# Kernel optimization log

Measured on AMD Instinct MI355X. Metric: run time of the kernel, lower is better.

## Reference

```python
import jax, jax.numpy as jnp
import numpy as np

T, B, D, Hd = 512, 64, 1024, 1024
SIGMA = 0.01


def setup_inputs() -> dict:
    key = jax.random.key(0)
    ks = jax.random.split(key, 9)
    inp = {
        "inputs": jax.random.normal(ks[0], (T, B, D), dtype=jnp.float32),
        "H0": jnp.zeros((B, Hd), dtype=jnp.float32),
        "C0": jnp.zeros((B, Hd), dtype=jnp.float32),
    }
    names_x = ["W_xi", "W_xf", "W_xo", "W_xc"]
    names_h = ["W_hi", "W_hf", "W_ho", "W_hc"]
    for i, n in enumerate(names_x):
        inp[n] = jax.random.normal(ks[1 + i], (D, Hd), dtype=jnp.float32) * SIGMA
    for i, n in enumerate(names_h):
        inp[n] = jax.random.normal(ks[5 + i], (Hd, Hd), dtype=jnp.float32) * SIGMA
    for n in ["b_i", "b_f", "b_o", "b_c"]:
        inp[n] = jnp.zeros((Hd,), dtype=jnp.float32)
    return inp


def reference(inputs, H0, C0, W_xi, W_xf, W_xo, W_xc,
              W_hi, W_hf, W_ho, W_hc, b_i, b_f, b_o, b_c):
    # Fuse the 4 input-projection and 4 hidden-projection GEMMs into 2 GEMMs
    # per step (same math as 8 separate matmuls, just concatenated).
    Wx = jnp.concatenate([W_xi, W_xf, W_xo, W_xc], axis=1)   # [D, 4H]
    Wh = jnp.concatenate([W_hi, W_hf, W_ho, W_hc], axis=1)   # [H, 4H]
    b = jnp.concatenate([b_i, b_f, b_o, b_c], axis=0)        # [4H]
    nh = b_i.shape[0]

    def step(carry, X):
        H, C = carry
        gates = X @ Wx + H @ Wh + b                          # [B, 4H]
        i, f, o, g = jnp.split(gates, 4, axis=1)
        I = jax.nn.sigmoid(i)
        F = jax.nn.sigmoid(f)
        O = jax.nn.sigmoid(o)
        C_tilde = jnp.tanh(g)
        C_new = F * C + I * C_tilde
        H_new = O * jnp.tanh(C_new)
        return (H_new, C_new), H_new

    (H_f, C_f), outputs = jax.lax.scan(step, (H0, C0), inputs)  # outputs [T, B, H]
    return outputs, (H_f, C_f)
```

## Files before the change

### kernel.cpp

```cpp
#include <hip/hip_runtime.h>
#include <cstdint>

#define TT 512
#define BB 64
#define DD 1024
#define HH 1024
#define NWG 128

typedef __attribute__((ext_vector_type(8))) __bf16 bf16x8;
typedef __attribute__((ext_vector_type(4))) float f32x4;

#define WS_XQ    0
#define WS_WHB   67108864ULL
#define WS_HQ    83886080ULL
#define WS_FLAGS 151126016ULL
#define FLAGS_BYTES ((TT + 1) * NWG * 4)

__device__ __forceinline__ unsigned short f2bf(float f) {
    unsigned int u = __float_as_uint(f);
    u = (u + 0x7fffu + ((u >> 16) & 1u)) >> 16;
    return (unsigned short)u;
}

__device__ __forceinline__ float sigm(float x) {
    return 1.0f / (1.0f + __expf(-x));
}
__device__ __forceinline__ float tanh_f(float x) {
    float a = fabsf(x);
    float e = __expf(-2.0f * a);
    float t = (1.0f - e) / (1.0f + e);
    return copysignf(t, x);
}

__device__ __forceinline__ unsigned long long pack4bf(float a, float b, float c, float d) {
    return (unsigned long long)f2bf(a)
         | ((unsigned long long)f2bf(b) << 16)
         | ((unsigned long long)f2bf(c) << 32)
         | ((unsigned long long)f2bf(d) << 48);
}

__global__ void cvt_x(const float* __restrict__ X, unsigned short* __restrict__ Xq) {
    int i = blockIdx.x * blockDim.x + threadIdx.x;
    const int n8 = TT * BB * DD / 8;
    if (i >= n8) return;
    const float4* s = (const float4*)X;
    float4 a = s[2 * i], b = s[2 * i + 1];
    union { unsigned short u[8]; uint4 q; } r;
    r.u[0] = f2bf(a.x); r.u[1] = f2bf(a.y); r.u[2] = f2bf(a.z); r.u[3] = f2bf(a.w);
    r.u[4] = f2bf(b.x); r.u[5] = f2bf(b.y); r.u[6] = f2bf(b.z); r.u[7] = f2bf(b.w);
    ((uint4*)Xq)[i] = r.q;
}

__global__ void pack_w(const float* __restrict__ Wxi, const float* __restrict__ Wxf,
                       const float* __restrict__ Wxo, const float* __restrict__ Wxc,
                       const float* __restrict__ Whi, const float* __restrict__ Whf,
                       const float* __restrict__ Who, const float* __restrict__ Whc,
                       unsigned short* __restrict__ WhB) {
    int tid = blockIdx.x * blockDim.x + threadIdx.x;
    int lane = tid & 63;
    int ct   = (tid >> 6) & 1;
    int s    = (tid >> 7) & 15;
    int kq   = (tid >> 11) & 3;
    int wg   = tid >> 13;
    int col  = ct * 16 + (lane & 15);
    int gate = col >> 3;
    int h    = wg * 8 + (col & 7);
    int kb   = kq * 512 + s * 32 + ((lane >> 4) & 3) * 8;

    const float* Wx[4] = {Wxi, Wxf, Wxo, Wxc};
    const float* Wh[4] = {Whi, Whf, Who, Whc};
    const float* W = (kb < 1024) ? (Wx[gate] + (size_t)kb * HH + h)
                                 : (Wh[gate] + (size_t)(kb - 1024) * HH + h);
    union { unsigned short u[8]; uint4 q; } r;
#pragma unroll
    for (int m = 0; m < 8; ++m) r.u[m] = f2bf(W[(size_t)m * HH]);
    *(uint4*)(WhB + (size_t)tid * 8) = r.q;
}

__global__ void __launch_bounds__(512, 2)
lstm_seq(const unsigned short* __restrict__ Xq, const unsigned short* __restrict__ WhB,
         unsigned short* __restrict__ Hq, int* flags,
         const float* __restrict__ H0, const float* __restrict__ C0,
         const float* __restrict__ bi, const float* __restrict__ bfp,
         const float* __restrict__ bo, const float* __restrict__ bc,
         float* __restrict__ out) {
    __shared__ float gpart[4][64][37];
    __shared__ int hs;

    const int wg    = blockIdx.x;
    const int tid   = threadIdx.x;
    const int wv    = tid >> 6;
    const int lane  = tid & 63;
    const int quad  = lane >> 4;
    const int l15   = lane & 15;
    const int rhalf = wv & 1;
    const bool isH  = (wv >= 4);
    const int kq    = isH ? 2 + ((wv - 4) >> 1) : (wv >> 1);
    const int arow0 = rhalf * 32 + l15;

    const bool isAct = (wv == 4) || (wv == 5);
    const int aidx   = tid - 256;
    const int r2     = aidx >> 1;
    const int ahalf  = aidx & 1;
    const int hcol0  = wg * 8 + ahalf * 4;

    float Bi[4], Bf[4], Bo[4], Bc[4], Cr[4];
    if (isAct) {
#pragma unroll
        for (int j = 0; j < 4; ++j) {
            Bi[j] = bi[hcol0 + j];
            Bf[j] = bfp[hcol0 + j];
            Bo[j] = bo[hcol0 + j];
            Bc[j] = bc[hcol0 + j];
            Cr[j] = C0[(size_t)r2 * HH + hcol0 + j];
        }
    }

    bf16x8 Breg[16][2];
    {
        const unsigned short* wp = WhB + (size_t)(wg * 4 + kq) * (16 * 2 * 64 * 8);
#pragma unroll
        for (int s = 0; s < 16; ++s)
#pragma unroll
            for (int ct = 0; ct < 2; ++ct)
                Breg[s][ct] = *(const bf16x8*)(wp + ((s * 2 + ct) * 64 + lane) * 8);
    }

    if (tid == 0) hs = 0;
    if (tid < 64) {
        const float* s = H0 + (size_t)tid * HH + wg * 8;
        unsigned long long a = pack4bf(s[0], s[1], s[2], s[3]);
        unsigned long long b = pack4bf(s[4], s[5], s[6], s[7]);
        unsigned long long* d = (unsigned long long*)(Hq + (size_t)tid * HH + wg * 8);
        __hip_atomic_store(d,     a, __ATOMIC_RELAXED, __HIP_MEMORY_SCOPE_AGENT);
        __hip_atomic_store(d + 1, b, __ATOMIC_RELAXED, __HIP_MEMORY_SCOPE_AGENT);
    }
    __syncthreads();
    if (tid == 0)
        __hip_atomic_store(&flags[wg], 1, __ATOMIC_RELAXED, __HIP_MEMORY_SCOPE_AGENT);

    for (int t = 0; t < TT; ++t) {
        f32x4 a00 = {0.f,0.f,0.f,0.f}, a01 = {0.f,0.f,0.f,0.f};
        f32x4 a10 = {0.f,0.f,0.f,0.f}, a11 = {0.f,0.f,0.f,0.f};

        if (!isH) {
            const unsigned short* xb = Xq + ((size_t)(t * BB + arow0)) * DD + kq * 512 + quad * 8;
#pragma unroll
            for (int s = 0; s < 16; ++s) {
                bf16x8 af0 = *(const bf16x8*)(xb + s * 32);
                bf16x8 af1 = *(const bf16x8*)(xb + 16 * DD + s * 32);
                a00 = __builtin_amdgcn_mfma_f32_16x16x32_bf16(af0, Breg[s][0], a00, 0, 0, 0);
                a01 = __builtin_amdgcn_mfma_f32_16x16x32_bf16(af0, Breg[s][1], a01, 0, 0, 0);
                a10 = __builtin_amdgcn_mfma_f32_16x16x32_bf16(af1, Breg[s][0], a10, 0, 0, 0);
                a11 = __builtin_amdgcn_mfma_f32_16x16x32_bf16(af1, Breg[s][1], a11, 0, 0, 0);
            }
        } else {
            const int kqh = kq - 2;
            const int* fp = flags + (size_t)t * NWG + kqh * 64 + lane;
            const unsigned short* hb = Hq + ((size_t)(t * BB + arow0)) * HH + kqh * 512 + quad * 8;
            int myf = 0;
            unsigned long long got = 0;

            while ((got & 0xFFFFFFFFull) != 0xFFFFFFFFull) {
                if (!myf) myf = __hip_atomic_load(fp, __ATOMIC_RELAXED, __HIP_MEMORY_SCOPE_AGENT);
                got = __ballot(myf != 0);
                if ((got & 0xFFFFFFFFull) != 0xFFFFFFFFull) __builtin_amdgcn_s_sleep(1);
            }
            asm volatile("" ::: "memory");
            bf16x8 af[8][2];
#pragma unroll
            for (int s = 0; s < 8; ++s) {
                af[s][0] = *(const bf16x8*)(hb + s * 32);
                af[s][1] = *(const bf16x8*)(hb + 16 * HH + s * 32);
            }
#pragma unroll
            for (int s = 0; s < 8; ++s) {
                a00 = __builtin_amdgcn_mfma_f32_16x16x32_bf16(af[s][0], Breg[s][0], a00, 0, 0, 0);
                a01 = __builtin_amdgcn_mfma_f32_16x16x32_bf16(af[s][0], Breg[s][1], a01, 0, 0, 0);
                a10 = __builtin_amdgcn_mfma_f32_16x16x32_bf16(af[s][1], Breg[s][0], a10, 0, 0, 0);
                a11 = __builtin_amdgcn_mfma_f32_16x16x32_bf16(af[s][1], Breg[s][1], a11, 0, 0, 0);
            }

            while (got != ~0ull) {
                if (!myf) myf = __hip_atomic_load(fp, __ATOMIC_RELAXED, __HIP_MEMORY_SCOPE_AGENT);
                got = __ballot(myf != 0);
                if (got != ~0ull) __builtin_amdgcn_s_sleep(1);
            }
            asm volatile("" ::: "memory");
#pragma unroll
            for (int s = 0; s < 8; ++s) {
                af[s][0] = *(const bf16x8*)(hb + (8 + s) * 32);
                af[s][1] = *(const bf16x8*)(hb + 16 * HH + (8 + s) * 32);
            }
#pragma unroll
            for (int s = 0; s < 8; ++s) {
                a00 = __builtin_amdgcn_mfma_f32_16x16x32_bf16(af[s][0], Breg[8 + s][0], a00, 0, 0, 0);
                a01 = __builtin_amdgcn_mfma_f32_16x16x32_bf16(af[s][0], Breg[8 + s][1], a01, 0, 0, 0);
                a10 = __builtin_amdgcn_mfma_f32_16x16x32_bf16(af[s][1], Breg[8 + s][0], a10, 0, 0, 0);
                a11 = __builtin_amdgcn_mfma_f32_16x16x32_bf16(af[s][1], Breg[8 + s][1], a11, 0, 0, 0);
            }
        }

#pragma unroll
        for (int r = 0; r < 4; ++r) {
            int row0 = rhalf * 32 + quad * 4 + r;
            gpart[kq][row0][l15]           = a00[r];
            gpart[kq][row0][16 + l15]      = a01[r];
            gpart[kq][row0 + 16][l15]      = a10[r];
            gpart[kq][row0 + 16][16 + l15] = a11[r];
        }
        __syncthreads();

        if (isAct) {
            float hv[4];
#pragma unroll
            for (int j = 0; j < 4; ++j) {
                const int c = ahalf * 4 + j;
                float gi = gpart[0][r2][c]      + gpart[1][r2][c]
                         + gpart[2][r2][c]      + gpart[3][r2][c]      + Bi[j];
                float gf = gpart[0][r2][8 + c]  + gpart[1][r2][8 + c]
                         + gpart[2][r2][8 + c]  + gpart[3][r2][8 + c]  + Bf[j];
                float go = gpart[0][r2][16 + c] + gpart[1][r2][16 + c]
                         + gpart[2][r2][16 + c] + gpart[3][r2][16 + c] + Bo[j];
                float gc = gpart[0][r2][24 + c] + gpart[1][r2][24 + c]
                         + gpart[2][r2][24 + c] + gpart[3][r2][24 + c] + Bc[j];
                float I = sigm(gi), F = sigm(gf), O = sigm(go), G = tanh_f(gc);
                Cr[j] = F * Cr[j] + I * G;
                hv[j] = O * tanh_f(Cr[j]);
            }
            unsigned long long pk = pack4bf(hv[0], hv[1], hv[2], hv[3]);
            __hip_atomic_store(
                (unsigned long long*)(Hq + ((size_t)(t + 1) * BB + r2) * HH + hcol0),
                pk, __ATOMIC_RELAXED, __HIP_MEMORY_SCOPE_AGENT);
            asm volatile("s_waitcnt vmcnt(0)" ::: "memory");
            if (lane == 0) {
                int prev = atomicAdd(&hs, 1);
                if (prev & 1)
                    __hip_atomic_store(flags + (size_t)(t + 1) * NWG + wg, 1,
                                       __ATOMIC_RELAXED, __HIP_MEMORY_SCOPE_AGENT);
            }
            float4 v = make_float4(hv[0], hv[1], hv[2], hv[3]);
            *(float4*)(out + ((size_t)t * BB + r2) * HH + hcol0) = v;
            if (t == TT - 1) {
                *(float4*)(out + (size_t)TT * BB * HH + (size_t)r2 * HH + hcol0) = v;
            }
        }
        __syncthreads();
    }

    if (isAct) {
        float* cf = out + (size_t)TT * BB * HH + (size_t)BB * HH;
        *(float4*)(cf + (size_t)r2 * HH + hcol0) = make_float4(Cr[0], Cr[1], Cr[2], Cr[3]);
    }
}

extern "C" void kernel_launch(void* const* d_in, const int* in_sizes, int n_in,
                              void* d_out, int out_size, void* d_ws, size_t ws_size,
                              hipStream_t stream) {
    const float* X   = (const float*)d_in[0];
    const float* H0  = (const float*)d_in[1];
    const float* C0  = (const float*)d_in[2];
    const float* Wxi = (const float*)d_in[3];
    const float* Wxf = (const float*)d_in[4];
    const float* Wxo = (const float*)d_in[5];
    const float* Wxc = (const float*)d_in[6];
    const float* Whi = (const float*)d_in[7];
    const float* Whf = (const float*)d_in[8];
    const float* Who = (const float*)d_in[9];
    const float* Whc = (const float*)d_in[10];
    const float* bi  = (const float*)d_in[11];
    const float* bf_ = (const float*)d_in[12];
    const float* bo  = (const float*)d_in[13];
    const float* bc  = (const float*)d_in[14];

    char* ws = (char*)d_ws;
    unsigned short* Xq  = (unsigned short*)(ws + WS_XQ);
    unsigned short* WhB = (unsigned short*)(ws + WS_WHB);
    unsigned short* Hq  = (unsigned short*)(ws + WS_HQ);
    int* flags          = (int*)(ws + WS_FLAGS);

    hipMemsetAsync(flags, 0, FLAGS_BYTES, stream);

    hipLaunchKernelGGL(cvt_x, dim3(TT * BB * DD / 8 / 256), dim3(256), 0, stream, X, Xq);
    hipLaunchKernelGGL(pack_w, dim3(4096), dim3(256), 0, stream,
                       Wxi, Wxf, Wxo, Wxc, Whi, Whf, Who, Whc, WhB);
    hipLaunchKernelGGL(lstm_seq, dim3(NWG), dim3(512), 0, stream,
                       Xq, WhB, Hq, flags, H0, C0, bi, bf_, bo, bc, (float*)d_out);
}
```

Measured before the change: 5.561 ms.

## Replace per-step flag handshake with sentinel-valued hidden-state polling

Removes the per-timestep flags array and its release protocol (waitcnt plus LDS counter plus flag store). Consumers instead poll the bf16 hidden-state words directly, using an all-ones sentinel written by a memset over the whole Hq buffer. This takes a store-then-flag round trip off the serial recurrence critical path. In exchange it adds a memset of about 67 MB before every launch and more atomic polling loads. It also relies on a valid h value never packing to the all-ones bit pattern, which is a NaN pattern in bf16.

```diff
diff --git a/kernel.cpp b/kernel.cpp
--- a/kernel.cpp
+++ b/kernel.cpp
@@ -13,8 +13,7 @@
 #define WS_XQ    0
 #define WS_WHB   67108864ULL
 #define WS_HQ    83886080ULL
-#define WS_FLAGS 151126016ULL
-#define FLAGS_BYTES ((TT + 1) * NWG * 4)
+#define HQ_BYTES ((size_t)(TT + 1) * BB * HH * 2)
 
 __device__ __forceinline__ unsigned short f2bf(float f) {
     unsigned int u = __float_as_uint(f);
@@ -79,13 +78,12 @@
 
 __global__ void __launch_bounds__(512, 2)
 lstm_seq(const unsigned short* __restrict__ Xq, const unsigned short* __restrict__ WhB,
-         unsigned short* __restrict__ Hq, int* flags,
+         unsigned short* __restrict__ Hq,
          const float* __restrict__ H0, const float* __restrict__ C0,
          const float* __restrict__ bi, const float* __restrict__ bfp,
          const float* __restrict__ bo, const float* __restrict__ bc,
          float* __restrict__ out) {
     __shared__ float gpart[4][64][37];
-    __shared__ int hs;
 
     const int wg    = blockIdx.x;
     const int tid   = threadIdx.x;
@@ -126,7 +124,6 @@
                 Breg[s][ct] = *(const bf16x8*)(wp + ((s * 2 + ct) * 64 + lane) * 8);
     }
 
-    if (tid == 0) hs = 0;
     if (tid < 64) {
         const float* s = H0 + (size_t)tid * HH + wg * 8;
         unsigned long long a = pack4bf(s[0], s[1], s[2], s[3]);
@@ -135,9 +132,8 @@
         __hip_atomic_store(d,     a, __ATOMIC_RELAXED, __HIP_MEMORY_SCOPE_AGENT);
         __hip_atomic_store(d + 1, b, __ATOMIC_RELAXED, __HIP_MEMORY_SCOPE_AGENT);
     }
-    __syncthreads();
-    if (tid == 0)
-        __hip_atomic_store(&flags[wg], 1, __ATOMIC_RELAXED, __HIP_MEMORY_SCOPE_AGENT);
+
+    const unsigned long long SENT = ~0ull;
 
     for (int t = 0; t < TT; ++t) {
         f32x4 a00 = {0.f,0.f,0.f,0.f}, a01 = {0.f,0.f,0.f,0.f};
@@ -156,48 +152,48 @@
             }
         } else {
             const int kqh = kq - 2;
-            const int* fp = flags + (size_t)t * NWG + kqh * 64 + lane;
             const unsigned short* hb = Hq + ((size_t)(t * BB + arow0)) * HH + kqh * 512 + quad * 8;
-            int myf = 0;
-            unsigned long long got = 0;
-
-            while ((got & 0xFFFFFFFFull) != 0xFFFFFFFFull) {
-                if (!myf) myf = __hip_atomic_load(fp, __ATOMIC_RELAXED, __HIP_MEMORY_SCOPE_AGENT);
-                got = __ballot(myf != 0);
-                if ((got & 0xFFFFFFFFull) != 0xFFFFFFFFull) __builtin_amdgcn_s_sleep(1);
-            }
-            asm volatile("" ::: "memory");
-            bf16x8 af[8][2];
-#pragma unroll
-            for (int s = 0; s < 8; ++s) {
-                af[s][0] = *(const bf16x8*)(hb + s * 32);
-                af[s][1] = *(const bf16x8*)(hb + 16 * HH + s * 32);
-            }
-#pragma unroll
-            for (int s = 0; s < 8; ++s) {
-                a00 = __builtin_amdgcn_mfma_f32_16x16x32_bf16(af[s][0], Breg[s][0], a00, 0, 0, 0);
-                a01 = __builtin_amdgcn_mfma_f32_16x16x32_bf16(af[s][0], Breg[s][1], a01, 0, 0, 0);
-                a10 = __builtin_amdgcn_mfma_f32_16x16x32_bf16(af[s][1], Breg[s][0], a10, 0, 0, 0);
-                a11 = __builtin_amdgcn_mfma_f32_16x16x32_bf16(af[s][1], Breg[s][1], a11, 0, 0, 0);
-            }
-
-            while (got != ~0ull) {
-                if (!myf) myf = __hip_atomic_load(fp, __ATOMIC_RELAXED, __HIP_MEMORY_SCOPE_AGENT);
-                got = __ballot(myf != 0);
-                if (got != ~0ull) __builtin_amdgcn_s_sleep(1);
-            }
-            asm volatile("" ::: "memory");
-#pragma unroll
-            for (int s = 0; s < 8; ++s) {
-                af[s][0] = *(const bf16x8*)(hb + (8 + s) * 32);
-                af[s][1] = *(const bf16x8*)(hb + 16 * HH + (8 + s) * 32);
-            }
-#pragma unroll
-            for (int s = 0; s < 8; ++s) {
-                a00 = __builtin_amdgcn_mfma_f32_16x16x32_bf16(af[s][0], Breg[8 + s][0], a00, 0, 0, 0);
-                a01 = __builtin_amdgcn_mfma_f32_16x16x32_bf16(af[s][0], Breg[8 + s][1], a01, 0, 0, 0);
-                a10 = __builtin_amdgcn_mfma_f32_16x16x32_bf16(af[s][1], Breg[8 + s][0], a10, 0, 0, 0);
-                a11 = __builtin_amdgcn_mfma_f32_16x16x32_bf16(af[s][1], Breg[8 + s][1], a11, 0, 0, 0);
+#pragma unroll
+            for (int p = 0; p < 2; ++p) {
+                unsigned long long vv[8][2][2];
+#pragma unroll
+                for (int s = 0; s < 8; ++s) {
+                    const unsigned long long* b0 =
+                        (const unsigned long long*)(hb + (p * 8 + s) * 32);
+                    const unsigned long long* b1 =
+                        (const unsigned long long*)(hb + 16 * HH + (p * 8 + s) * 32);
+                    vv[s][0][0] = __hip_atomic_load(b0,     __ATOMIC_RELAXED, __HIP_MEMORY_SCOPE_AGENT);
+                    vv[s][0][1] = __hip_atomic_load(b0 + 1, __ATOMIC_RELAXED, __HIP_MEMORY_SCOPE_AGENT);
+                    vv[s][1][0] = __hip_atomic_load(b1,     __ATOMIC_RELAXED, __HIP_MEMORY_SCOPE_AGENT);
+                    vv[s][1][1] = __hip_atomic_load(b1 + 1, __ATOMIC_RELAXED, __HIP_MEMORY_SCOPE_AGENT);
+                }
+                bool any;
+                do {
+                    any = false;
+#pragma unroll
+                    for (int s = 0; s < 8; ++s)
+#pragma unroll
+                        for (int rt = 0; rt < 2; ++rt)
+#pragma unroll
+                            for (int h = 0; h < 2; ++h)
+                                if (vv[s][rt][h] == SENT) {
+                                    const unsigned long long* b = (const unsigned long long*)
+                                        (hb + rt * 16 * HH + (p * 8 + s) * 32) + h;
+                                    vv[s][rt][h] = __hip_atomic_load(
+                                        b, __ATOMIC_RELAXED, __HIP_MEMORY_SCOPE_AGENT);
+                                    any = true;
+                                }
+                } while (any);
+#pragma unroll
+                for (int s = 0; s < 8; ++s) {
+                    union { unsigned long long u[2]; bf16x8 v; } f0, f1;
+                    f0.u[0] = vv[s][0][0]; f0.u[1] = vv[s][0][1];
+                    f1.u[0] = vv[s][1][0]; f1.u[1] = vv[s][1][1];
+                    a00 = __builtin_amdgcn_mfma_f32_16x16x32_bf16(f0.v, Breg[p*8+s][0], a00, 0, 0, 0);
+                    a01 = __builtin_amdgcn_mfma_f32_16x16x32_bf16(f0.v, Breg[p*8+s][1], a01, 0, 0, 0);
+                    a10 = __builtin_amdgcn_mfma_f32_16x16x32_bf16(f1.v, Breg[p*8+s][0], a10, 0, 0, 0);
+                    a11 = __builtin_amdgcn_mfma_f32_16x16x32_bf16(f1.v, Breg[p*8+s][1], a11, 0, 0, 0);
+                }
             }
         }
 
@@ -232,13 +228,6 @@
             __hip_atomic_store(
                 (unsigned long long*)(Hq + ((size_t)(t + 1) * BB + r2) * HH + hcol0),
                 pk, __ATOMIC_RELAXED, __HIP_MEMORY_SCOPE_AGENT);
-            asm volatile("s_waitcnt vmcnt(0)" ::: "memory");
-            if (lane == 0) {
-                int prev = atomicAdd(&hs, 1);
-                if (prev & 1)
-                    __hip_atomic_store(flags + (size_t)(t + 1) * NWG + wg, 1,
-                                       __ATOMIC_RELAXED, __HIP_MEMORY_SCOPE_AGENT);
-            }
             float4 v = make_float4(hv[0], hv[1], hv[2], hv[3]);
             *(float4*)(out + ((size_t)t * BB + r2) * HH + hcol0) = v;
             if (t == TT - 1) {
@@ -277,13 +266,12 @@
     unsigned short* Xq  = (unsigned short*)(ws + WS_XQ);
     unsigned short* WhB = (unsigned short*)(ws + WS_WHB);
     unsigned short* Hq  = (unsigned short*)(ws + WS_HQ);
-    int* flags          = (int*)(ws + WS_FLAGS);
-
-    hipMemsetAsync(flags, 0, FLAGS_BYTES, stream);
+
+    hipMemsetAsync(Hq, 0xFF, HQ_BYTES, stream);
 
     hipLaunchKernelGGL(cvt_x, dim3(TT * BB * DD / 8 / 256), dim3(256), 0, stream, X, Xq);
     hipLaunchKernelGGL(pack_w, dim3(4096), dim3(256), 0, stream,
                        Wxi, Wxf, Wxo, Wxc, Whi, Whf, Who, Whc, WhB);
     hipLaunchKernelGGL(lstm_seq, dim3(NWG), dim3(512), 0, stream,
-                       Xq, WhB, Hq, flags, H0, C0, bi, bf_, bo, bc, (float*)d_out);
-}
+                       Xq, WhB, Hq, H0, C0, bi, bf_, bo, bc, (float*)d_out);
+}
```

After: 6.924 ms. 24.5% more time.

## Use per-wave monotonic ring-buffer flags for finer-grained cross-workgroup step sync

Applied to the files above, without the earlier changes.

Each of the two activation waves now publishes its own flag, set to a monotonically increasing step value in an 8-slot ring padded to 16 bytes per flag. This replaces the shared-memory atomic counter that made the second wave publish for both. Consumer waves poll only the half of the rows they actually need, and compare against a step threshold instead of testing for nonzero. This shortens the critical path of the per-step cross-workgroup handoff and shrinks the flag buffer to clear. It also drops the gpart row padding from 37 to 36 and removes an initial __syncthreads, which risks LDS bank conflicts and relies on the ring never being lapped.

```diff
diff --git a/kernel.cpp b/kernel.cpp
--- a/kernel.cpp
+++ b/kernel.cpp
@@ -14,7 +14,7 @@
 #define WS_WHB   67108864ULL
 #define WS_HQ    83886080ULL
 #define WS_FLAGS 151126016ULL
-#define FLAGS_BYTES ((TT + 1) * NWG * 4)
+#define FLAGS_BYTES (256 * 128)
 
 __device__ __forceinline__ unsigned short f2bf(float f) {
     unsigned int u = __float_as_uint(f);
@@ -84,8 +84,7 @@
          const float* __restrict__ bi, const float* __restrict__ bfp,
          const float* __restrict__ bo, const float* __restrict__ bc,
          float* __restrict__ out) {
-    __shared__ float gpart[4][64][37];
-    __shared__ int hs;
+    __shared__ float gpart[4][64][36];
 
     const int wg    = blockIdx.x;
     const int tid   = threadIdx.x;
@@ -126,7 +125,6 @@
                 Breg[s][ct] = *(const bf16x8*)(wp + ((s * 2 + ct) * 64 + lane) * 8);
     }
 
-    if (tid == 0) hs = 0;
     if (tid < 64) {
         const float* s = H0 + (size_t)tid * HH + wg * 8;
         unsigned long long a = pack4bf(s[0], s[1], s[2], s[3]);
@@ -135,9 +133,12 @@
         __hip_atomic_store(d,     a, __ATOMIC_RELAXED, __HIP_MEMORY_SCOPE_AGENT);
         __hip_atomic_store(d + 1, b, __ATOMIC_RELAXED, __HIP_MEMORY_SCOPE_AGENT);
     }
-    __syncthreads();
-    if (tid == 0)
-        __hip_atomic_store(&flags[wg], 1, __ATOMIC_RELAXED, __HIP_MEMORY_SCOPE_AGENT);
+    if (wv == 0) {
+        asm volatile("s_waitcnt vmcnt(0)" ::: "memory");
+        if (lane < 2)
+            __hip_atomic_store(flags + ((wg * 2 + lane) * 8 + 0) * 4, 1,
+                               __ATOMIC_RELAXED, __HIP_MEMORY_SCOPE_AGENT);
+    }
 
     for (int t = 0; t < TT; ++t) {
         f32x4 a00 = {0.f,0.f,0.f,0.f}, a01 = {0.f,0.f,0.f,0.f};
@@ -155,49 +156,58 @@
                 a11 = __builtin_amdgcn_mfma_f32_16x16x32_bf16(af1, Breg[s][1], a11, 0, 0, 0);
             }
         } else {
-            const int kqh = kq - 2;
-            const int* fp = flags + (size_t)t * NWG + kqh * 64 + lane;
+            const int kqh  = kq - 2;
+            const int slot = t & 7;
+            const int thr  = t + 1;
+            const int* fp  = flags + (((kqh * 64 + lane) * 2 + rhalf) * 8 + slot) * 4;
             const unsigned short* hb = Hq + ((size_t)(t * BB + arow0)) * HH + kqh * 512 + quad * 8;
-            int myf = 0;
-            unsigned long long got = 0;
-
+
+            int myf = __hip_atomic_load(fp, __ATOMIC_RELAXED, __HIP_MEMORY_SCOPE_AGENT);
+            unsigned long long got = __ballot(myf >= thr);
             while ((got & 0xFFFFFFFFull) != 0xFFFFFFFFull) {
-                if (!myf) myf = __hip_atomic_load(fp, __ATOMIC_RELAXED, __HIP_MEMORY_SCOPE_AGENT);
-                got = __ballot(myf != 0);
-                if ((got & 0xFFFFFFFFull) != 0xFFFFFFFFull) __builtin_amdgcn_s_sleep(1);
+                __builtin_amdgcn_s_sleep(2);
+                if (myf < thr)
+                    myf = __hip_atomic_load(fp, __ATOMIC_RELAXED, __HIP_MEMORY_SCOPE_AGENT);
+                got = __ballot(myf >= thr);
             }
             asm volatile("" ::: "memory");
-            bf16x8 af[8][2];
-#pragma unroll
-            for (int s = 0; s < 8; ++s) {
-                af[s][0] = *(const bf16x8*)(hb + s * 32);
-                af[s][1] = *(const bf16x8*)(hb + 16 * HH + s * 32);
-            }
-#pragma unroll
-            for (int s = 0; s < 8; ++s) {
-                a00 = __builtin_amdgcn_mfma_f32_16x16x32_bf16(af[s][0], Breg[s][0], a00, 0, 0, 0);
-                a01 = __builtin_amdgcn_mfma_f32_16x16x32_bf16(af[s][0], Breg[s][1], a01, 0, 0, 0);
-                a10 = __builtin_amdgcn_mfma_f32_16x16x32_bf16(af[s][1], Breg[s][0], a10, 0, 0, 0);
-                a11 = __builtin_amdgcn_mfma_f32_16x16x32_bf16(af[s][1], Breg[s][1], a11, 0, 0, 0);
+            {
+                bf16x8 af[8][2];
+#pragma unroll
+                for (int s = 0; s < 8; ++s) {
+                    af[s][0] = *(const bf16x8*)(hb + s * 32);
+                    af[s][1] = *(const bf16x8*)(hb + 16 * HH + s * 32);
+                }
+#pragma unroll
+                for (int s = 0; s < 8; ++s) {
+                    a00 = __builtin_amdgcn_mfma_f32_16x16x32_bf16(af[s][0], Breg[s][0], a00, 0, 0, 0);
+                    a01 = __builtin_amdgcn_mfma_f32_16x16x32_bf16(af[s][0], Breg[s][1], a01, 0, 0, 0);
+                    a10 = __builtin_amdgcn_mfma_f32_16x16x32_bf16(af[s][1], Breg[s][0], a10, 0, 0, 0);
+                    a11 = __builtin_amdgcn_mfma_f32_16x16x32_bf16(af[s][1], Breg[s][1], a11, 0, 0, 0);
+                }
             }
 
             while (got != ~0ull) {
-                if (!myf) myf = __hip_atomic_load(fp, __ATOMIC_RELAXED, __HIP_MEMORY_SCOPE_AGENT);
-                got = __ballot(myf != 0);
-                if (got != ~0ull) __builtin_amdgcn_s_sleep(1);
+                __builtin_amdgcn_s_sleep(2);
+                if (myf < thr)
+                    myf = __hip_atomic_load(fp, __ATOMIC_RELAXED, __HIP_MEMORY_SCOPE_AGENT);
+                got = __ballot(myf >= thr);
             }
             asm volatile("" ::: "memory");
-#pragma unroll
-            for (int s = 0; s < 8; ++s) {
-                af[s][0] = *(const bf16x8*)(hb + (8 + s) * 32);
-                af[s][1] = *(const bf16x8*)(hb + 16 * HH + (8 + s) * 32);
-            }
-#pragma unroll
-            for (int s = 0; s < 8; ++s) {
-                a00 = __builtin_amdgcn_mfma_f32_16x16x32_bf16(af[s][0], Breg[8 + s][0], a00, 0, 0, 0);
-                a01 = __builtin_amdgcn_mfma_f32_16x16x32_bf16(af[s][0], Breg[8 + s][1], a01, 0, 0, 0);
-                a10 = __builtin_amdgcn_mfma_f32_16x16x32_bf16(af[s][1], Breg[8 + s][0], a10, 0, 0, 0);
-                a11 = __builtin_amdgcn_mfma_f32_16x16x32_bf16(af[s][1], Breg[8 + s][1], a11, 0, 0, 0);
+            {
+                bf16x8 af[8][2];
+#pragma unroll
+                for (int s = 0; s < 8; ++s) {
+                    af[s][0] = *(const bf16x8*)(hb + (8 + s) * 32);
+                    af[s][1] = *(const bf16x8*)(hb + 16 * HH + (8 + s) * 32);
+                }
+#pragma unroll
+                for (int s = 0; s < 8; ++s) {
+                    a00 = __builtin_amdgcn_mfma_f32_16x16x32_bf16(af[s][0], Breg[8 + s][0], a00, 0, 0, 0);
+                    a01 = __builtin_amdgcn_mfma_f32_16x16x32_bf16(af[s][0], Breg[8 + s][1], a01, 0, 0, 0);
+                    a10 = __builtin_amdgcn_mfma_f32_16x16x32_bf16(af[s][1], Breg[8 + s][0], a10, 0, 0, 0);
+                    a11 = __builtin_amdgcn_mfma_f32_16x16x32_bf16(af[s][1], Breg[8 + s][1], a11, 0, 0, 0);
+                }
             }
         }
 
@@ -233,12 +243,10 @@
                 (unsigned long long*)(Hq + ((size_t)(t + 1) * BB + r2) * HH + hcol0),
                 pk, __ATOMIC_RELAXED, __HIP_MEMORY_SCOPE_AGENT);
             asm volatile("s_waitcnt vmcnt(0)" ::: "memory");
-            if (lane == 0) {
-                int prev = atomicAdd(&hs, 1);
-                if (prev & 1)
-                    __hip_atomic_store(flags + (size_t)(t + 1) * NWG + wg, 1,
-                                       __ATOMIC_RELAXED, __HIP_MEMORY_SCOPE_AGENT);
-            }
+            if (lane == 0)
+                __hip_atomic_store(
+                    flags + ((wg * 2 + (wv - 4)) * 8 + ((t + 1) & 7)) * 4, t + 2,
+                    __ATOMIC_RELAXED, __HIP_MEMORY_SCOPE_AGENT);
             float4 v = make_float4(hv[0], hv[1], hv[2], hv[3]);
             *(float4*)(out + ((size_t)t * BB + r2) * HH + hcol0) = v;
             if (t == TT - 1) {
```

Measured after the change: 5.024 ms. -9.7%, faster.
